# Kernel optimization log

Hardware: AMD Instinct MI355X
Metric: run time of the kernel (lower is better)

Reference implementation:

```python
import jax, jax.numpy as jnp
import numpy as np

EPS = 1e-5

def conv3x3(x, w, b=None):
    # NCHW, OIHW, stride 1, padding 1
    y = jax.lax.conv_general_dilated(x, w, (1, 1), ((1, 1), (1, 1)),
                                     dimension_numbers=('NCHW', 'OIHW', 'NCHW'))
    if b is not None:
        y = y + b[None, :, None, None]
    return y

def batchnorm(x, g, b):
    # training-mode BN (PyTorch default): biased variance over (N,H,W)
    m = x.mean((0, 2, 3), keepdims=True)
    v = x.var((0, 2, 3), keepdims=True)
    return (x - m) * jax.lax.rsqrt(v + EPS) * g[None, :, None, None] + b[None, :, None, None]

def upsample2x_align_corners(x):
    # bilinear, align_corners=True, scale_factor=2
    def lerp_axis(a, Lin, axis):
        Lout = 2 * Lin
        c = jnp.arange(Lout, dtype=a.dtype) * (Lin - 1) / (Lout - 1)
        i0 = jnp.floor(c).astype(jnp.int32)
        i1 = jnp.minimum(i0 + 1, Lin - 1)
        w = c - i0.astype(a.dtype)
        shape = [1] * a.ndim
        shape[axis] = Lout
        w = w.reshape(shape)
        return jnp.take(a, i0, axis=axis) * (1 - w) + jnp.take(a, i1, axis=axis) * w
    x = lerp_axis(x, x.shape[2], 2)
    x = lerp_axis(x, x.shape[3], 3)
    return x

def deform_sample(x, offsets):
    # torchvision DeformConv2d v1 sampling: kernel 3x3, pad 1, offsets [B,18,H,W]
    # layout: per kernel point k (row-major), channels (2k, 2k+1) = (dy, dx)
    B, C, H, W = x.shape
    K = 9
    off = offsets.reshape(B, K, 2, H, W)
    ky, kx = jnp.meshgrid(jnp.arange(3) - 1, jnp.arange(3) - 1, indexing='ij')
    ky = ky.reshape(K).astype(x.dtype)
    kx = kx.reshape(K).astype(x.dtype)
    gy = jnp.arange(H, dtype=x.dtype)[None, None, :, None]
    gx = jnp.arange(W, dtype=x.dtype)[None, None, None, :]
    py = gy + ky[None, :, None, None] + off[:, :, 0]  # [B,K,H,W]
    px = gx + kx[None, :, None, None] + off[:, :, 1]
    y0 = jnp.floor(py)
    x0 = jnp.floor(px)
    wy = (py - y0)[:, None]  # [B,1,K,H,W]
    wx = (px - x0)[:, None]
    y0i = y0.astype(jnp.int32)
    x0i = x0.astype(jnp.int32)
    x_flat = x.reshape(B, C, H * W)
    def gather(yi, xi):
        valid = ((yi >= 0) & (yi < H) & (xi >= 0) & (xi < W))
        idx = jnp.clip(yi, 0, H - 1) * W + jnp.clip(xi, 0, W - 1)  # [B,K,H,W]
        g = jnp.take_along_axis(x_flat, idx.reshape(B, 1, K * H * W), axis=2)
        return g.reshape(B, C, K, H, W) * valid[:, None].astype(x.dtype)
    v00 = gather(y0i, x0i)
    v01 = gather(y0i, x0i + 1)
    v10 = gather(y0i + 1, x0i)
    v11 = gather(y0i + 1, x0i + 1)
    return (v00 * (1 - wy) * (1 - wx) + v01 * (1 - wy) * wx
            + v10 * wy * (1 - wx) + v11 * wy * wx)

def setup_inputs() -> dict:
    key = jax.random.key(0)
    ks = jax.random.split(key, 6)
    B, in_ch, skip_ch, out_ch = 4, 256, 128, 128
    Hs, Ws = 128, 128
    x = jax.random.normal(ks[0], (B, in_ch, Hs // 2, Ws // 2), jnp.float32)
    skip = jax.random.normal(ks[1], (B, skip_ch, Hs, Ws), jnp.float32)
    cat_ch = in_ch + skip_ch
    conv1_w = jax.random.normal(ks[2], (out_ch, cat_ch, 3, 3), jnp.float32) * (2.0 / (cat_ch * 9)) ** 0.5
    off_w = jax.random.normal(ks[3], (18, out_ch, 3, 3), jnp.float32) * 0.01
    off_b = jnp.zeros((18,), jnp.float32)
    def_w = jax.random.normal(ks[4], (out_ch, out_ch, 3, 3), jnp.float32) * (2.0 / (out_ch * 9)) ** 0.5
    def_b = jnp.zeros((out_ch,), jnp.float32)
    return {
        'x': x, 'skip': skip,
        'conv1_w': conv1_w,
        'bn1_g': jnp.ones((out_ch,), jnp.float32), 'bn1_b': jnp.zeros((out_ch,), jnp.float32),
        'off_w': off_w, 'off_b': off_b,
        'def_w': def_w, 'def_b': def_b,
        'bn2_g': jnp.ones((out_ch,), jnp.float32), 'bn2_b': jnp.zeros((out_ch,), jnp.float32),
    }

def reference(x, skip, conv1_w, bn1_g, bn1_b, off_w, off_b, def_w, def_b, bn2_g, bn2_b):
    xu = upsample2x_align_corners(x)
    dh = skip.shape[2] - xu.shape[2]
    dw = skip.shape[3] - xu.shape[3]
    if dh != 0 or dw != 0:
        xu = jnp.pad(xu, ((0, 0), (0, 0), (dh // 2, dh - dh // 2), (dw // 2, dw - dw // 2)))
    cat = jnp.concatenate([skip, xu], axis=1)
    h = jax.nn.relu(batchnorm(conv3x3(cat, conv1_w), bn1_g, bn1_b))
    offsets = conv3x3(h, off_w, off_b)  # [B,18,H,W]
    sampled = deform_sample(h, offsets)  # [B,C,9,H,W]
    O = def_w.shape[0]
    y = jnp.einsum('ock,bckhw->bohw', def_w.reshape(O, def_w.shape[1], 9), sampled)
    y = y + def_b[None, :, None, None]
    return jax.nn.relu(batchnorm(y, bn2_g, bn2_b))
```

## Files before the change

kernel.cpp:

```cpp
#include <hip/hip_runtime.h>
#include <hip/hip_bf16.h>

typedef __hip_bfloat16 bf16;
typedef __bf16 bf16x8 __attribute__((ext_vector_type(8)));
typedef __bf16 bf16x4 __attribute__((ext_vector_type(4)));
typedef float  f32x4  __attribute__((ext_vector_type(4)));

constexpr int NB   = 4;
constexpr int H    = 128;
constexpr int W    = 128;
constexpr int HW   = H * W;
constexpr int NPIX = NB * HW;
constexpr int CCAT = 384;
constexpr int CSKIP= 128;
constexpr int CIN  = 256;
constexpr int CO   = 128;
constexpr int HS   = 64;
constexpr int WP   = 130;
constexpr int K1   = 3456;
constexpr int KD   = 1152;
constexpr int NBORD= 2 * WP + 2 * (WP - 2);
constexpr float EPS = 1e-5f;

__device__ __forceinline__ float b2f(bf16 v){ return __bfloat162float(v); }
__device__ __forceinline__ bf16  f2b(float v){ return __float2bfloat16(v); }

__device__ __forceinline__ void async_copy16(const void* g, void* s){
    __builtin_amdgcn_global_load_lds((const __attribute__((address_space(1))) void*)g,
                                     (__attribute__((address_space(3))) void*)s, 16, 0, 0);
}

__device__ __forceinline__ void border_yx(int p, int& y, int& x){
    if (p < WP)             { y = 0;        x = p; }
    else if (p < 2 * WP)    { y = WP - 1;   x = p - WP; }
    else if (p < 2 * WP + (WP - 2)) { y = p - 2 * WP + 1;          x = 0; }
    else                    { y = p - (2 * WP + (WP - 2)) + 1;     x = WP - 1; }
}

__global__ void k_prep(float* __restrict__ sums, bf16* __restrict__ catp,
                       bf16* __restrict__ hp){
    int i = blockIdx.x * blockDim.x + threadIdx.x;
    int stride = gridDim.x * blockDim.x;
    for (int j = i; j < 512; j += stride) sums[j] = 0.f;
    const int nCat = NB * NBORD * CCAT;
    for (int j = i; j < nCat; j += stride){
        int c = j % CCAT, r = j / CCAT, p = r % NBORD, b = r / NBORD;
        int y, x; border_yx(p, y, x);
        catp[(((size_t)b * WP + y) * WP + x) * CCAT + c] = f2b(0.f);
    }
    const int nHp = NB * NBORD * CO;
    for (int j = i; j < nHp; j += stride){
        int c = j % CO, r = j / CO, p = r % NBORD, b = r / NBORD;
        int y, x; border_yx(p, y, x);
        hp[(((size_t)b * WP + y) * WP + x) * CO + c] = f2b(0.f);
    }
}

__global__ __launch_bounds__(256) void k_build_cat2(const float* __restrict__ x,
                                                    const float* __restrict__ skip,
                                                    bf16* __restrict__ catp){
    constexpr int TS = 66;
    __shared__ bf16 tile[128 * TS];
    int t  = threadIdx.x;
    int y  = blockIdx.x % H, b = blockIdx.x / H;
    int xx = t & 127, cp = t >> 7;

    float cy = (y * 63.0f) / 127.0f;
    int   y0 = (int)cy;
    int   y1 = min(y0 + 1, HS - 1);
    float wy = cy - y0;
    float cxf = (xx * 63.0f) / 127.0f;
    int   x0 = (int)cxf;
    int   x1 = min(x0 + 1, HS - 1);
    float wx = cxf - x0;

    bf16* orow = catp + (((size_t)b * WP + y + 1) * WP + 1) * CCAT;

    for (int chunk = 0; chunk < 6; chunk++){
        int cbase = chunk * 64;
        if (chunk >= 1) __syncthreads();
        if (chunk < 2){
            const float* sb = skip + ((size_t)(b * CSKIP + cbase + cp * 32) * H + y) * W;
#pragma unroll
            for (int i = 0; i < 32; i++)
                tile[xx * TS + cp * 32 + i] = f2b(sb[(size_t)i * HW + xx]);
        } else {
            int icb = (chunk - 2) * 64 + cp * 32;
            const float* xr0 = x + ((size_t)(b * CIN + icb) * HS + y0) * HS;
            const float* xr1 = x + ((size_t)(b * CIN + icb) * HS + y1) * HS;
#pragma unroll
            for (int i = 0; i < 32; i++){
                const float* r0 = xr0 + (size_t)i * HS * HS;
                const float* r1 = xr1 + (size_t)i * HS * HS;
                float v0 = r0[x0] * (1 - wx) + r0[x1] * wx;
                float v1 = r1[x0] * (1 - wx) + r1[x1] * wx;
                tile[xx * TS + cp * 32 + i] = f2b(v0 * (1 - wy) + v1 * wy);
            }
        }
        __syncthreads();
        int cc2 = (t & 31) * 2;
        int px0 = t >> 5;
#pragma unroll
        for (int pp = 0; pp < 16; pp++){
            int px = pp * 8 + px0;
            unsigned int v = *(const unsigned int*)&tile[px * TS + cc2];
            *(unsigned int*)&orow[(size_t)px * CCAT + cbase + cc2] = v;
        }
    }
}

__global__ void k_tr_all(const float* __restrict__ w1, const float* __restrict__ wo,
                         const float* __restrict__ wd,
                         bf16* __restrict__ wt1, bf16* __restrict__ wto,
                         bf16* __restrict__ wtd){
    int i = blockIdx.x * blockDim.x + threadIdx.x;
    if (i < CO * K1){
        int e  = i & 7;
        int l  = (i >> 3) & 63;
        int nb = (i >> 9) & 7;
        int ks = (i >> 12) & 1;
        int p  = i >> 13;
        int gp = p / 6, q = p - gp * 6;
        int ky = gp / 3, ci = gp - ky * 3;
        int kx = q >> 1, s64 = q & 1;
        int oc = nb * 16 + (l & 15);
        int ic = ci * 128 + s64 * 64 + ks * 32 + (l >> 4) * 8 + e;
        wt1[i] = f2b(w1[((oc * CCAT + ic) * 3 + ky) * 3 + kx]);
        return;
    }
    i -= CO * K1;
    if (i < 32 * KD){
        int e  = i & 7;
        int l  = (i >> 3) & 63;
        int wn = (i >> 9) & 1;
        int s  = (i >> 10) & 3;
        int kk = i >> 12;
        int ky = kk / 3, kx = kk - ky * 3;
        int oc = wn * 16 + (l & 15);
        int ic = s * 32 + (l >> 4) * 8 + e;
        wto[i] = (oc < 18) ? f2b(wo[((oc * CO + ic) * 3 + ky) * 3 + kx]) : f2b(0.f);
        return;
    }
    i -= 32 * KD;
    if (i < CO * KD){
        int e  = i & 7;
        int l  = (i >> 3) & 63;
        int ni = (i >> 9) & 3;
        int wn = (i >> 11) & 1;
        int ks = (i >> 12) & 1;
        int kc = i >> 13;
        int oc = wn * 64 + ni * 16 + (l & 15);
        int ic = (kc & 1) * 64 + ks * 32 + (l >> 4) * 8 + e;
        int kp = kc >> 1;
        wtd[i] = f2b(wd[(oc * CO + ic) * 9 + kp]);
    }
}

__global__ __launch_bounds__(256) void k_conv1_mfma(const bf16* __restrict__ catp,
                                                    const bf16* __restrict__ wbt,
                                                    bf16* __restrict__ hp,
                                                    float* __restrict__ sums){
    __shared__ unsigned short Ab[2][68 * 128];
    __shared__ float ps[256];
    int t = threadIdx.x;
    int l = t & 63, w = t >> 6;
    int half = blockIdx.x & 1;
    int y = (blockIdx.x >> 1) % H, b = blockIdx.x / (2 * H);
    int px0 = half * 64;

    int m = l & 15, quad = l >> 4;

    f32x4 acc[4][2];
#pragma unroll
    for (int i = 0; i < 4; i++)
#pragma unroll
        for (int j = 0; j < 2; j++) acc[i][j] = f32x4{0.f, 0.f, 0.f, 0.f};

    const size_t rowStride = (size_t)WP * CCAT;
    const char* wq = (const char*)wbt + w * 2048 + l * 16;

    bf16x8 bA[2][2], bB[2][2];

    {
        const bf16* Arow = catp + ((size_t)(b * WP) + y) * rowStride + (size_t)px0 * CCAT;
        for (int i = w; i < 17; i += 4){
            int G = i * 64 + l;
            int px = G >> 4, ol = G & 15;
            int osrc = ol ^ (px & 7);
            async_copy16(Arow + (size_t)px * CCAT + osrc * 8, &Ab[0][i * 512]);
        }
#pragma unroll
        for (int ks = 0; ks < 2; ks++)
#pragma unroll
            for (int ni = 0; ni < 2; ni++)
                bA[ks][ni] = *(const bf16x8*)(wq + ks * 8192 + ni * 1024);
    }
    __syncthreads();

#pragma unroll 1
    for (int g = 0; g < 9; g++){
        if (g < 8){
            int gn = g + 1;
            int kyn = gn / 3, cin = gn - kyn * 3;
            const bf16* Arow = catp + ((size_t)(b * WP) + y + kyn) * rowStride
                             + (size_t)px0 * CCAT + cin * 128;
            for (int i = w; i < 17; i += 4){
                int G = i * 64 + l;
                int px = G >> 4, ol = G & 15;
                int osrc = ol ^ (px & 7);
                async_copy16(Arow + (size_t)px * CCAT + osrc * 8, &Ab[gn & 1][i * 512]);
            }
        }
        const bf16x8* ap = (const bf16x8*)&Ab[g & 1][0];
        const char* wg = wq + (size_t)g * 6 * 16384;
#pragma unroll
        for (int j = 0; j < 6; j++){
            int kx = j >> 1, s64 = j & 1;
            const char* wnx = wg + (j + 1) * 16384;
            if (j & 1){
#pragma unroll
                for (int ks = 0; ks < 2; ks++)
#pragma unroll
                    for (int ni = 0; ni < 2; ni++)
                        bA[ks][ni] = *(const bf16x8*)(wnx + ks * 8192 + ni * 1024);
            } else {
#pragma unroll
                for (int ks = 0; ks < 2; ks++)
#pragma unroll
                    for (int ni = 0; ni < 2; ni++)
                        bB[ks][ni] = *(const bf16x8*)(wnx + ks * 8192 + ni * 1024);
            }
#pragma unroll
            for (int ks = 0; ks < 2; ks++){
                int s = s64 * 2 + ks;
                bf16x8 af[4];
#pragma unroll
                for (int mi = 0; mi < 4; mi++){
                    int pxk = mi * 16 + m + kx;
                    af[mi] = ap[pxk * 16 + ((s * 4 + quad) ^ (pxk & 7))];
                }
                if (j & 1){
#pragma unroll
                    for (int mi = 0; mi < 4; mi++)
#pragma unroll
                        for (int ni = 0; ni < 2; ni++)
                            acc[mi][ni] = __builtin_amdgcn_mfma_f32_16x16x32_bf16(
                                af[mi], bB[ks][ni], acc[mi][ni], 0, 0, 0);
                } else {
#pragma unroll
                    for (int mi = 0; mi < 4; mi++)
#pragma unroll
                        for (int ni = 0; ni < 2; ni++)
                            acc[mi][ni] = __builtin_amdgcn_mfma_f32_16x16x32_bf16(
                                af[mi], bA[ks][ni], acc[mi][ni], 0, 0, 0);
                }
            }
        }
        __syncthreads();
    }

    size_t obase = (((size_t)b * WP + y + 1) * WP + 1 + px0) * CO;
#pragma unroll
    for (int mi = 0; mi < 4; mi++){
        int p0 = mi * 16 + quad * 4;
#pragma unroll
        for (int ni = 0; ni < 2; ni++){
            int oc = w * 32 + ni * 16 + m;
#pragma unroll
            for (int r = 0; r < 4; r++)
                hp[obase + (size_t)(p0 + r) * CO + oc] = f2b(acc[mi][ni][r]);
        }
    }
    ps[t] = 0.f;
    __syncthreads();
#pragma unroll
    for (int ni = 0; ni < 2; ni++){
        int ch = w * 32 + ni * 16 + m;
        float s = 0.f, q2 = 0.f;
#pragma unroll
        for (int mi = 0; mi < 4; mi++)
#pragma unroll
            for (int r = 0; r < 4; r++){
                float v = acc[mi][ni][r];
                s += v; q2 += v * v;
            }
        s += __shfl_xor(s, 16); s += __shfl_xor(s, 32);
        q2 += __shfl_xor(q2, 16); q2 += __shfl_xor(q2, 32);
        if (quad == 0){
            atomicAdd(&ps[ch], s);
            atomicAdd(&ps[128 + ch], q2);
        }
    }
    __syncthreads();
    if (t < 128){
        atomicAdd(&sums[t],       ps[t]);
        atomicAdd(&sums[128 + t], ps[128 + t]);
    }
}

__global__ __launch_bounds__(256) void k_bn_apply_pad(bf16* __restrict__ t,
                                                      const float* __restrict__ sums,
                                                      const float* __restrict__ g,
                                                      const float* __restrict__ bb){
    __shared__ float ssc[256];
    int tt = threadIdx.x;
    if (tt < 128){
        float mean = sums[tt] / (float)NPIX;
        float var  = sums[128 + tt] / (float)NPIX - mean * mean;
        float scale = g[tt] * rsqrtf(var + EPS);
        ssc[tt]       = scale;
        ssc[128 + tt] = bb[tt] - mean * scale;
    }
    __syncthreads();
    int i = blockIdx.x * 256 + tt;
    if (i >= NPIX * CO) return;
    int c = i & 127;
    int pix = i >> 7;
    int xw = pix & 127, yh = (pix >> 7) & 127, b = pix >> 14;
    size_t a = (((size_t)b * WP + yh + 1) * WP + xw + 1) * CO + c;
    float v = b2f(t[a]) * ssc[c] + ssc[128 + c];
    t[a] = f2b(v > 0.f ? v : 0.f);
}

__global__ __launch_bounds__(256) void k_conv_off_mfma(const bf16* __restrict__ hp,
                                                       const bf16* __restrict__ wob,
                                                       const float* __restrict__ off_b,
                                                       bf16* __restrict__ offs){
    __shared__ unsigned short Ab[68 * 128];
    int t = threadIdx.x, l = t & 63, w = t >> 6;
    int half = blockIdx.x & 1;
    int y = (blockIdx.x >> 1) % H, b = blockIdx.x / (2 * H);
    int px0 = half * 64;
    int m = l & 15, quad = l >> 4;
    int wm = w & 1, wn = w >> 1;

    f32x4 acc[2];
#pragma unroll
    for (int i = 0; i < 2; i++) acc[i] = f32x4{0.f, 0.f, 0.f, 0.f};

    const size_t rowStrideH = (size_t)WP * CO;
    const char* wq = (const char*)wob + wn * 1024 + l * 16;

    for (int ky = 0; ky < 3; ky++){
        if (ky) __syncthreads();
        const bf16* Arow = hp + ((size_t)(b * WP) + y + ky) * rowStrideH
                         + (size_t)px0 * CO;
        for (int i = w; i < 17; i += 4){
            int G  = i * 64 + l;
            int px = G >> 4, ol = G & 15;
            int osrc = ol ^ (px & 7);
            async_copy16(Arow + (size_t)px * CO + osrc * 8, &Ab[i * 512]);
        }
        bf16x8 bfr[3][4];
#pragma unroll
        for (int kx = 0; kx < 3; kx++)
#pragma unroll
            for (int s = 0; s < 4; s++)
                bfr[kx][s] = *(const bf16x8*)(wq + (((ky * 3 + kx) * 4 + s) * 2048));
        __syncthreads();
        const bf16x8* ap = (const bf16x8*)Ab;
        for (int kx = 0; kx < 3; kx++){
#pragma unroll
            for (int s = 0; s < 4; s++){
#pragma unroll
                for (int mi = 0; mi < 2; mi++){
                    int pxk = wm * 32 + mi * 16 + m + kx;
                    bf16x8 af = ap[pxk * 16 + ((s * 4 + quad) ^ (pxk & 7))];
                    acc[mi] = __builtin_amdgcn_mfma_f32_16x16x32_bf16(af, bfr[kx][s], acc[mi], 0, 0, 0);
                }
            }
        }
    }
    int oc = wn * 16 + m;
    if (oc < 18){
        float bias = off_b[oc];
        int rowpix = b * HW + y * W + px0;
#pragma unroll
        for (int mi = 0; mi < 2; mi++){
            int p0 = wm * 32 + mi * 16 + quad * 4;
#pragma unroll
            for (int r = 0; r < 4; r++)
                offs[(size_t)(rowpix + p0 + r) * 18 + oc] = f2b(acc[mi][r] + bias);
        }
    }
}

__global__ __launch_bounds__(256) void k_deform_mfma(const bf16* __restrict__ hp,
                                                     const bf16* __restrict__ offs,
                                                     const bf16* __restrict__ wdb,
                                                     const float* __restrict__ def_b,
                                                     bf16* __restrict__ y,
                                                     float* __restrict__ sums){
    __shared__ unsigned short Ab[2][128 * 64];
    __shared__ int2   sc_yx[9 * 128];
    __shared__ float4 sc_w[9 * 128];
    __shared__ float  ps[256];

    int t = threadIdx.x, l = t & 63, w = t >> 6;
    int yrow = blockIdx.x % H, b = blockIdx.x / H;
    int rowpix = b * HW + yrow * W;

    for (int idx = t; idx < 9 * 128; idx += 256){
        int kp = idx >> 7, px = idx & 127;
        float dy = b2f(offs[(size_t)(rowpix + px) * 18 + 2 * kp]);
        float dx = b2f(offs[(size_t)(rowpix + px) * 18 + 2 * kp + 1]);
        float py = yrow + (kp / 3 - 1) + dy;
        float pxx = px + (kp % 3 - 1) + dx;
        float fy = floorf(py), fx = floorf(pxx);
        float wy = py - fy, wx = pxx - fx;
        int y0 = (int)fy, x0 = (int)fx;
        bool vy0 = (y0 >= 0) && (y0 < H);
        bool vy1 = (y0 + 1 >= 0) && (y0 + 1 < H);
        bool vx0 = (x0 >= 0) && (x0 < W);
        bool vx1 = (x0 + 1 >= 0) && (x0 + 1 < W);
        int y0c = min(max(y0, 0), H - 1),     y1c = min(max(y0 + 1, 0), H - 1);
        int x0c = min(max(x0, 0), W - 1),     x1c = min(max(x0 + 1, 0), W - 1);
        sc_yx[idx] = make_int2(((y0c + 1) * WP) | (((y1c + 1) * WP) << 16),
                               (x0c + 1) | ((x1c + 1) << 16));
        sc_w[idx] = make_float4((1 - wy) * (1 - wx) * (float)(vy0 && vx0),
                                (1 - wy) * wx       * (float)(vy0 && vx1),
                                wy * (1 - wx)       * (float)(vy1 && vx0),
                                wy * wx             * (float)(vy1 && vx1));
    }
    __syncthreads();

    int m = l & 15, quad = l >> 4;
    int wm = w & 1, wn = w >> 1;
    int g = l >> 4, j = l & 15;

    f32x4 acc[4][4];
#pragma unroll
    for (int i = 0; i < 4; i++)
#pragma unroll
        for (int jj = 0; jj < 4; jj++) acc[i][jj] = f32x4{0.f, 0.f, 0.f, 0.f};

    const bf16* hpb = hp + (size_t)b * WP * WP * CO;
    const char* wq = (const char*)wdb + wn * 4096 + l * 16;

    auto GEN = [&](int kc, unsigned short* dst){
        int kp = kc >> 1, ch = (kc & 1) * 64;
        int cb = ch + j * 4;
#pragma unroll
        for (int p = 0; p < 8; p++){
            int px = w * 32 + g * 8 + p;
            int idx = kp * 128 + px;
            int2 yx = sc_yx[idx];
            float4 w4 = sc_w[idx];
            int r0 = yx.x & 0xffff, r1 = ((unsigned)yx.x) >> 16;
            int c0 = yx.y & 0xffff, c1 = ((unsigned)yx.y) >> 16;
            const bf16* base = hpb + cb;
            bf16x4 s00 = *(const bf16x4*)(base + (size_t)(r0 + c0) * CO);
            bf16x4 s01 = *(const bf16x4*)(base + (size_t)(r0 + c1) * CO);
            bf16x4 s10 = *(const bf16x4*)(base + (size_t)(r1 + c0) * CO);
            bf16x4 s11 = *(const bf16x4*)(base + (size_t)(r1 + c1) * CO);
            bf16x4 pv;
#pragma unroll
            for (int r = 0; r < 4; r++){
                float v = w4.x * (float)s00[r] + w4.y * (float)s01[r]
                        + w4.z * (float)s10[r] + w4.w * (float)s11[r];
                pv[r] = (__bf16)v;
            }
            int oct_sw = (j >> 1) ^ (px & 7);
            *(bf16x4*)&dst[px * 64 + oct_sw * 8 + (j & 1) * 4] = pv;
        }
    };

    GEN(0, &Ab[0][0]);

#pragma unroll 1
    for (int kc = 0; kc < 18; kc++){
        __syncthreads();
        bf16x8 bfr[2][4];
        const char* wk = wq + (size_t)kc * 16384;
#pragma unroll
        for (int ks = 0; ks < 2; ks++)
#pragma unroll
            for (int ni = 0; ni < 4; ni++)
                bfr[ks][ni] = *(const bf16x8*)(wk + ks * 8192 + ni * 1024);
        if (kc < 17) GEN(kc + 1, &Ab[(kc + 1) & 1][0]);

        const bf16x8* ap = (const bf16x8*)&Ab[kc & 1][0];
#pragma unroll
        for (int ks = 0; ks < 2; ks++){
            bf16x8 af[4];
#pragma unroll
            for (int mi = 0; mi < 4; mi++){
                int px = wm * 64 + mi * 16 + m;
                af[mi] = ap[px * 8 + ((ks * 4 + quad) ^ (px & 7))];
            }
#pragma unroll
            for (int mi = 0; mi < 4; mi++)
#pragma unroll
                for (int ni = 0; ni < 4; ni++)
                    acc[mi][ni] = __builtin_amdgcn_mfma_f32_16x16x32_bf16(
                        af[mi], bfr[ks][ni], acc[mi][ni], 0, 0, 0);
        }
    }
#pragma unroll
    for (int mi = 0; mi < 4; mi++){
        int p0 = wm * 64 + mi * 16 + quad * 4;
#pragma unroll
        for (int ni = 0; ni < 4; ni++){
            int oc = wn * 64 + ni * 16 + m;
            float bias = def_b[oc];
#pragma unroll
            for (int r = 0; r < 4; r++)
                y[(size_t)(rowpix + p0 + r) * CO + oc] = f2b(acc[mi][ni][r] + bias);
        }
    }
    ps[t] = 0.f;
    __syncthreads();
#pragma unroll
    for (int ni = 0; ni < 4; ni++){
        int ch = wn * 64 + ni * 16 + m;
        float bias = def_b[ch];
        float s = 0.f, q = 0.f;
#pragma unroll
        for (int mi = 0; mi < 4; mi++)
#pragma unroll
            for (int r = 0; r < 4; r++){
                float v = acc[mi][ni][r] + bias;
                s += v; q += v * v;
            }
        s += __shfl_xor(s, 16); s += __shfl_xor(s, 32);
        q += __shfl_xor(q, 16); q += __shfl_xor(q, 32);
        if (quad == 0){
            atomicAdd(&ps[ch], s);
            atomicAdd(&ps[128 + ch], q);
        }
    }
    __syncthreads();
    if (t < 128){
        atomicAdd(&sums[t],       ps[t]);
        atomicAdd(&sums[128 + t], ps[128 + t]);
    }
}

__global__ __launch_bounds__(256) void k_final(const bf16* __restrict__ yb,
                                               const float* __restrict__ sums,
                                               const float* __restrict__ g,
                                               const float* __restrict__ bb,
                                               float* __restrict__ out){
    __shared__ unsigned short tile[128 * 129];
    __shared__ float ssc[256];
    int t = threadIdx.x;
    if (t < 128){
        float mean = sums[t] / (float)NPIX;
        float var  = sums[128 + t] / (float)NPIX - mean * mean;
        float scale = g[t] * rsqrtf(var + EPS);
        ssc[t]       = scale;
        ssc[128 + t] = bb[t] - mean * scale;
    }
    int yrow = blockIdx.x % H, b = blockIdx.x / H;
    int rowbase = b * HW + yrow * W;
    const unsigned short* src = (const unsigned short*)yb;
    for (int it = 0; it < 64; it++){
        int idx = it * 256 + t;
        int c = idx & 127, px = idx >> 7;
        tile[px * 129 + c] = src[(size_t)(rowbase + px) * CO + c];
    }
    __syncthreads();
    for (int it = 0; it < 64; it++){
        int idx = it * 256 + t;
        int xw = idx & 127, o = idx >> 7;
        unsigned short u = tile[xw * 129 + o];
        float v = (float)(*(const __bf16*)&u);
        v = v * ssc[o] + ssc[128 + o];
        out[(((size_t)b * CO + o) * H + yrow) * W + xw] = v > 0.f ? v : 0.f;
    }
}

extern "C" void kernel_launch(void* const* d_in, const int* in_sizes, int n_in,
                              void* d_out, int out_size, void* d_ws, size_t ws_size,
                              hipStream_t stream){
    const float* x      = (const float*)d_in[0];
    const float* skip   = (const float*)d_in[1];
    const float* conv1w = (const float*)d_in[2];
    const float* bn1g   = (const float*)d_in[3];
    const float* bn1b   = (const float*)d_in[4];
    const float* offw   = (const float*)d_in[5];
    const float* offb   = (const float*)d_in[6];
    const float* defw   = (const float*)d_in[7];
    const float* defb   = (const float*)d_in[8];
    const float* bn2g   = (const float*)d_in[9];
    const float* bn2b   = (const float*)d_in[10];
    float* out = (float*)d_out;

    char* ws = (char*)d_ws;
    size_t off_bytes = 0;
    auto alloc = [&](size_t bytes) -> void* {
        void* p = ws + off_bytes;
        off_bytes += (bytes + 255) & ~(size_t)255;
        return p;
    };
    const size_t catp_elems = (size_t)NB * WP * WP * CCAT;
    const size_t hp_elems   = (size_t)NB * WP * WP * CO;
    bf16*  catp  = (bf16*) alloc(catp_elems * 2 + 2048);
    bf16*  hp    = (bf16*) alloc(hp_elems * 2 + 2048);
    bf16*  offs  = (bf16*) alloc((size_t)NPIX * 18 * 2);
    bf16*  yb    = (bf16*) alloc((size_t)NPIX * CO * 2);
    bf16*  wbt   = (bf16*) alloc((size_t)CO * K1 * 2 + 32768);
    bf16*  wob   = (bf16*) alloc((size_t)32 * KD * 2);
    bf16*  wdb   = (bf16*) alloc((size_t)CO * KD * 2);
    float* sums  = (float*)alloc(512 * 4);
    float* sums1 = sums;
    float* sums2 = sums + 256;

    k_prep<<<1024, 256, 0, stream>>>(sums, catp, hp);

    k_build_cat2<<<NB * H, 256, 0, stream>>>(x, skip, catp);

    const int ntr = CO * K1 + 32 * KD + CO * KD;
    k_tr_all<<<(ntr + 255) / 256, 256, 0, stream>>>(conv1w, offw, defw, wbt, wob, wdb);

    k_conv1_mfma<<<NB * H * 2, 256, 0, stream>>>(catp, wbt, hp, sums1);

    k_bn_apply_pad<<<(NPIX * CO + 255) / 256, 256, 0, stream>>>(hp, sums1, bn1g, bn1b);

    k_conv_off_mfma<<<NB * H * 2, 256, 0, stream>>>(hp, wob, offb, offs);

    k_deform_mfma<<<NB * H, 256, 0, stream>>>(hp, offs, wdb, defb, yb, sums2);

    k_final<<<NB * H, 256, 0, stream>>>(yb, sums2, bn2g, bn2b, out);
}
```

Before: 332.6 us.

## Fuse BN1 apply into offset conv and merge setup kernels into one launch

Merges the prep, concat-build and weight-transpose kernels into a single setup launch. Removes the standalone BN1 apply pass: the offset convolution now normalizes and ReLUs the raw conv1 output while staging it into LDS, and writes the normalized center row to a new buffer that the deform kernel reads. It also widens the LDS XOR swizzle from 8 to 16 slots in both convs. This cuts launches and one full read-modify-write of the conv1 activation, at the cost of an extra workspace buffer, synchronous loads instead of async LDS copies in the offset conv, and the new buffer's border relying on zero-filled memory.

Measured after the change: 314.5 us (median of 2 runs). 1.06x faster.

```diff
diff --git a/kernel.cpp b/kernel.cpp
--- a/kernel.cpp
+++ b/kernel.cpp
@@ -22,6 +22,10 @@
 constexpr int NBORD= 2 * WP + 2 * (WP - 2);
 constexpr float EPS = 1e-5f;
 
+constexpr int NTR  = CO * K1 + 32 * KD + CO * KD;
+constexpr int NCATB= NB * NBORD * CCAT;
+constexpr int NHPB = NB * NBORD * CO;
+
 __device__ __forceinline__ float b2f(bf16 v){ return __bfloat162float(v); }
 __device__ __forceinline__ bf16  f2b(float v){ return __float2bfloat16(v); }
 
@@ -37,112 +41,101 @@
     else                    { y = p - (2 * WP + (WP - 2)) + 1;     x = WP - 1; }
 }
 
-__global__ void k_prep(float* __restrict__ sums, bf16* __restrict__ catp,
-                       bf16* __restrict__ hp){
-    int i = blockIdx.x * blockDim.x + threadIdx.x;
-    int stride = gridDim.x * blockDim.x;
-    for (int j = i; j < 512; j += stride) sums[j] = 0.f;
-    const int nCat = NB * NBORD * CCAT;
-    for (int j = i; j < nCat; j += stride){
-        int c = j % CCAT, r = j / CCAT, p = r % NBORD, b = r / NBORD;
-        int y, x; border_yx(p, y, x);
-        catp[(((size_t)b * WP + y) * WP + x) * CCAT + c] = f2b(0.f);
-    }
-    const int nHp = NB * NBORD * CO;
-    for (int j = i; j < nHp; j += stride){
-        int c = j % CO, r = j / CO, p = r % NBORD, b = r / NBORD;
-        int y, x; border_yx(p, y, x);
-        hp[(((size_t)b * WP + y) * WP + x) * CO + c] = f2b(0.f);
-    }
-}
-
-__global__ __launch_bounds__(256) void k_build_cat2(const float* __restrict__ x,
-                                                    const float* __restrict__ skip,
-                                                    bf16* __restrict__ catp){
+__global__ __launch_bounds__(256) void k_setup(const float* __restrict__ x,
+                                               const float* __restrict__ skip,
+                                               const float* __restrict__ w1,
+                                               const float* __restrict__ wo,
+                                               const float* __restrict__ wd,
+                                               float* __restrict__ sums,
+                                               bf16* __restrict__ catp,
+                                               bf16* __restrict__ hp,
+                                               bf16* __restrict__ wt1,
+                                               bf16* __restrict__ wto,
+                                               bf16* __restrict__ wtd){
     constexpr int TS = 66;
     __shared__ bf16 tile[128 * TS];
-    int t  = threadIdx.x;
-    int y  = blockIdx.x % H, b = blockIdx.x / H;
-    int xx = t & 127, cp = t >> 7;
-
-    float cy = (y * 63.0f) / 127.0f;
-    int   y0 = (int)cy;
-    int   y1 = min(y0 + 1, HS - 1);
-    float wy = cy - y0;
-    float cxf = (xx * 63.0f) / 127.0f;
-    int   x0 = (int)cxf;
-    int   x1 = min(x0 + 1, HS - 1);
-    float wx = cxf - x0;
-
-    bf16* orow = catp + (((size_t)b * WP + y + 1) * WP + 1) * CCAT;
-
-    for (int chunk = 0; chunk < 6; chunk++){
-        int cbase = chunk * 64;
-        if (chunk >= 1) __syncthreads();
-        if (chunk < 2){
-            const float* sb = skip + ((size_t)(b * CSKIP + cbase + cp * 32) * H + y) * W;
-#pragma unroll
-            for (int i = 0; i < 32; i++)
-                tile[xx * TS + cp * 32 + i] = f2b(sb[(size_t)i * HW + xx]);
-        } else {
-            int icb = (chunk - 2) * 64 + cp * 32;
-            const float* xr0 = x + ((size_t)(b * CIN + icb) * HS + y0) * HS;
-            const float* xr1 = x + ((size_t)(b * CIN + icb) * HS + y1) * HS;
-#pragma unroll
-            for (int i = 0; i < 32; i++){
-                const float* r0 = xr0 + (size_t)i * HS * HS;
-                const float* r1 = xr1 + (size_t)i * HS * HS;
-                float v0 = r0[x0] * (1 - wx) + r0[x1] * wx;
-                float v1 = r1[x0] * (1 - wx) + r1[x1] * wx;
-                tile[xx * TS + cp * 32 + i] = f2b(v0 * (1 - wy) + v1 * wy);
-            }
-        }
-        __syncthreads();
-        int cc2 = (t & 31) * 2;
-        int px0 = t >> 5;
-#pragma unroll
-        for (int pp = 0; pp < 16; pp++){
-            int px = pp * 8 + px0;
-            unsigned int v = *(const unsigned int*)&tile[px * TS + cc2];
-            *(unsigned int*)&orow[(size_t)px * CCAT + cbase + cc2] = v;
-        }
-    }
-}
-
-__global__ void k_tr_all(const float* __restrict__ w1, const float* __restrict__ wo,
-                         const float* __restrict__ wd,
-                         bf16* __restrict__ wt1, bf16* __restrict__ wto,
-                         bf16* __restrict__ wtd){
-    int i = blockIdx.x * blockDim.x + threadIdx.x;
-    if (i < CO * K1){
-        int e  = i & 7;
-        int l  = (i >> 3) & 63;
-        int nb = (i >> 9) & 7;
-        int ks = (i >> 12) & 1;
-        int p  = i >> 13;
-        int gp = p / 6, q = p - gp * 6;
-        int ky = gp / 3, ci = gp - ky * 3;
-        int kx = q >> 1, s64 = q & 1;
-        int oc = nb * 16 + (l & 15);
-        int ic = ci * 128 + s64 * 64 + ks * 32 + (l >> 4) * 8 + e;
-        wt1[i] = f2b(w1[((oc * CCAT + ic) * 3 + ky) * 3 + kx]);
+    int t = threadIdx.x;
+
+    if (blockIdx.x < NB * H){
+        int y  = blockIdx.x % H, b = blockIdx.x / H;
+        int xx = t & 127, cp = t >> 7;
+
+        float cy = (y * 63.0f) / 127.0f;
+        int   y0 = (int)cy;
+        int   y1 = min(y0 + 1, HS - 1);
+        float wy = cy - y0;
+        float cxf = (xx * 63.0f) / 127.0f;
+        int   x0 = (int)cxf;
+        int   x1 = min(x0 + 1, HS - 1);
+        float wx = cxf - x0;
+
+        bf16* orow = catp + (((size_t)b * WP + y + 1) * WP + 1) * CCAT;
+
+        for (int chunk = 0; chunk < 6; chunk++){
+            int cbase = chunk * 64;
+            if (chunk >= 1) __syncthreads();
+            if (chunk < 2){
+                const float* sb = skip + ((size_t)(b * CSKIP + cbase + cp * 32) * H + y) * W;
+#pragma unroll
+                for (int i = 0; i < 32; i++)
+                    tile[xx * TS + cp * 32 + i] = f2b(sb[(size_t)i * HW + xx]);
+            } else {
+                int icb = (chunk - 2) * 64 + cp * 32;
+                const float* xr0 = x + ((size_t)(b * CIN + icb) * HS + y0) * HS;
+                const float* xr1 = x + ((size_t)(b * CIN + icb) * HS + y1) * HS;
+#pragma unroll
+                for (int i = 0; i < 32; i++){
+                    const float* r0 = xr0 + (size_t)i * HS * HS;
+                    const float* r1 = xr1 + (size_t)i * HS * HS;
+                    float v0 = r0[x0] * (1 - wx) + r0[x1] * wx;
+                    float v1 = r1[x0] * (1 - wx) + r1[x1] * wx;
+                    tile[xx * TS + cp * 32 + i] = f2b(v0 * (1 - wy) + v1 * wy);
+                }
+            }
+            __syncthreads();
+            int cc2 = (t & 31) * 2;
+            int px0 = t >> 5;
+#pragma unroll
+            for (int pp = 0; pp < 16; pp++){
+                int px = pp * 8 + px0;
+                unsigned int v = *(const unsigned int*)&tile[px * TS + cc2];
+                *(unsigned int*)&orow[(size_t)px * CCAT + cbase + cc2] = v;
+            }
+        }
         return;
     }
-    i -= CO * K1;
-    if (i < 32 * KD){
-        int e  = i & 7;
-        int l  = (i >> 3) & 63;
-        int wn = (i >> 9) & 1;
-        int s  = (i >> 10) & 3;
-        int kk = i >> 12;
-        int ky = kk / 3, kx = kk - ky * 3;
-        int oc = wn * 16 + (l & 15);
-        int ic = s * 32 + (l >> 4) * 8 + e;
-        wto[i] = (oc < 18) ? f2b(wo[((oc * CO + ic) * 3 + ky) * 3 + kx]) : f2b(0.f);
-        return;
-    }
-    i -= 32 * KD;
-    if (i < CO * KD){
+
+    int idx = (blockIdx.x - NB * H) * 256 + t;
+    if (idx < NTR){
+        int i = idx;
+        if (i < CO * K1){
+            int e  = i & 7;
+            int l  = (i >> 3) & 63;
+            int nb = (i >> 9) & 7;
+            int ks = (i >> 12) & 1;
+            int p  = i >> 13;
+            int gp = p / 6, q = p - gp * 6;
+            int ky = gp / 3, ci = gp - ky * 3;
+            int kx = q >> 1, s64 = q & 1;
+            int oc = nb * 16 + (l & 15);
+            int ic = ci * 128 + s64 * 64 + ks * 32 + (l >> 4) * 8 + e;
+            wt1[i] = f2b(w1[((oc * CCAT + ic) * 3 + ky) * 3 + kx]);
+            return;
+        }
+        i -= CO * K1;
+        if (i < 32 * KD){
+            int e  = i & 7;
+            int l  = (i >> 3) & 63;
+            int wn = (i >> 9) & 1;
+            int s  = (i >> 10) & 3;
+            int kk = i >> 12;
+            int ky = kk / 3, kx = kk - ky * 3;
+            int oc = wn * 16 + (l & 15);
+            int ic = s * 32 + (l >> 4) * 8 + e;
+            wto[i] = (oc < 18) ? f2b(wo[((oc * CO + ic) * 3 + ky) * 3 + kx]) : f2b(0.f);
+            return;
+        }
+        i -= 32 * KD;
         int e  = i & 7;
         int l  = (i >> 3) & 63;
         int ni = (i >> 9) & 3;
@@ -153,6 +146,22 @@
         int ic = (kc & 1) * 64 + ks * 32 + (l >> 4) * 8 + e;
         int kp = kc >> 1;
         wtd[i] = f2b(wd[(oc * CO + ic) * 9 + kp]);
+        return;
+    }
+    idx -= NTR;
+    if (idx < 512){ sums[idx] = 0.f; return; }
+    idx -= 512;
+    if (idx < NCATB){
+        int c = idx % CCAT, r = idx / CCAT, p = r % NBORD, b = r / NBORD;
+        int y, xw; border_yx(p, y, xw);
+        catp[(((size_t)b * WP + y) * WP + xw) * CCAT + c] = f2b(0.f);
+        return;
+    }
+    idx -= NCATB;
+    if (idx < NHPB){
+        int c = idx % CO, r = idx / CO, p = r % NBORD, b = r / NBORD;
+        int y, xw; border_yx(p, y, xw);
+        hp[(((size_t)b * WP + y) * WP + xw) * CO + c] = f2b(0.f);
     }
 }
 
@@ -186,7 +195,7 @@
         for (int i = w; i < 17; i += 4){
             int G = i * 64 + l;
             int px = G >> 4, ol = G & 15;
-            int osrc = ol ^ (px & 7);
+            int osrc = ol ^ (px & 15);
             async_copy16(Arow + (size_t)px * CCAT + osrc * 8, &Ab[0][i * 512]);
         }
 #pragma unroll
@@ -207,7 +216,7 @@
             for (int i = w; i < 17; i += 4){
                 int G = i * 64 + l;
                 int px = G >> 4, ol = G & 15;
-                int osrc = ol ^ (px & 7);
+                int osrc = ol ^ (px & 15);
                 async_copy16(Arow + (size_t)px * CCAT + osrc * 8, &Ab[gn & 1][i * 512]);
             }
         }
@@ -237,7 +246,7 @@
 #pragma unroll
                 for (int mi = 0; mi < 4; mi++){
                     int pxk = mi * 16 + m + kx;
-                    af[mi] = ap[pxk * 16 + ((s * 4 + quad) ^ (pxk & 7))];
+                    af[mi] = ap[pxk * 16 + ((s * 4 + quad) ^ (pxk & 15))];
                 }
                 if (j & 1){
 #pragma unroll
@@ -298,36 +307,23 @@
     }
 }
 
-__global__ __launch_bounds__(256) void k_bn_apply_pad(bf16* __restrict__ t,
-                                                      const float* __restrict__ sums,
-                                                      const float* __restrict__ g,
-                                                      const float* __restrict__ bb){
-    __shared__ float ssc[256];
-    int tt = threadIdx.x;
-    if (tt < 128){
-        float mean = sums[tt] / (float)NPIX;
-        float var  = sums[128 + tt] / (float)NPIX - mean * mean;
-        float scale = g[tt] * rsqrtf(var + EPS);
-        ssc[tt]       = scale;
-        ssc[128 + tt] = bb[tt] - mean * scale;
-    }
-    __syncthreads();
-    int i = blockIdx.x * 256 + tt;
-    if (i >= NPIX * CO) return;
-    int c = i & 127;
-    int pix = i >> 7;
-    int xw = pix & 127, yh = (pix >> 7) & 127, b = pix >> 14;
-    size_t a = (((size_t)b * WP + yh + 1) * WP + xw + 1) * CO + c;
-    float v = b2f(t[a]) * ssc[c] + ssc[128 + c];
-    t[a] = f2b(v > 0.f ? v : 0.f);
-}
-
 __global__ __launch_bounds__(256) void k_conv_off_mfma(const bf16* __restrict__ hp,
                                                        const bf16* __restrict__ wob,
                                                        const float* __restrict__ off_b,
-                                                       bf16* __restrict__ offs){
+                                                       const float* __restrict__ sums,
+                                                       const float* __restrict__ bn_g,
+                                                       const float* __restrict__ bn_b,
+                                                       bf16* __restrict__ offs,
+                                                       bf16* __restrict__ hq){
     __shared__ unsigned short Ab[68 * 128];
+    __shared__ float2 ssc[128];
     int t = threadIdx.x, l = t & 63, w = t >> 6;
+    if (t < 128){
+        float mean = sums[t] / (float)NPIX;
+        float var  = sums[128 + t] / (float)NPIX - mean * mean;
+        float sc   = bn_g[t] * rsqrtf(var + EPS);
+        ssc[t] = make_float2(sc, bn_b[t] - mean * sc);
+    }
     int half = blockIdx.x & 1;
     int y = (blockIdx.x >> 1) % H, b = blockIdx.x / (2 * H);
     int px0 = half * 64;
@@ -340,16 +336,33 @@
 
     const size_t rowStrideH = (size_t)WP * CO;
     const char* wq = (const char*)wob + wn * 1024 + l * 16;
+    __syncthreads();
 
     for (int ky = 0; ky < 3; ky++){
         if (ky) __syncthreads();
-        const bf16* Arow = hp + ((size_t)(b * WP) + y + ky) * rowStrideH
+        int row = y + ky;
+        const bf16* Arow = hp + ((size_t)(b * WP) + row) * rowStrideH
                          + (size_t)px0 * CO;
+        bool rowborder = (row == 0) || (row == WP - 1);
+        bf16* hqrow = hq + ((size_t)(b * WP) + row) * rowStrideH;
         for (int i = w; i < 17; i += 4){
             int G  = i * 64 + l;
             int px = G >> 4, ol = G & 15;
-            int osrc = ol ^ (px & 7);
-            async_copy16(Arow + (size_t)px * CO + osrc * 8, &Ab[i * 512]);
+            int osrc = ol ^ (px & 15);
+            int col = px0 + px;
+            bool zero = rowborder || (col == 0) || (col >= WP - 1);
+            bf16x8 raw = *(const bf16x8*)(Arow + (size_t)px * CO + osrc * 8);
+            bf16x8 outv;
+#pragma unroll
+            for (int e = 0; e < 8; e++){
+                float2 sb = ssc[osrc * 8 + e];
+                float v = (float)raw[e] * sb.x + sb.y;
+                v = v > 0.f ? v : 0.f;
+                outv[e] = zero ? (__bf16)0.f : (__bf16)v;
+            }
+            *(bf16x8*)&Ab[G * 8] = outv;
+            if (ky == 1 && col >= 1 && col <= 128)
+                *(bf16x8*)(hqrow + (size_t)col * CO + osrc * 8) = outv;
         }
         bf16x8 bfr[3][4];
 #pragma unroll
@@ -365,7 +378,7 @@
 #pragma unroll
                 for (int mi = 0; mi < 2; mi++){
                     int pxk = wm * 32 + mi * 16 + m + kx;
-                    bf16x8 af = ap[pxk * 16 + ((s * 4 + quad) ^ (pxk & 7))];
+                    bf16x8 af = ap[pxk * 16 + ((s * 4 + quad) ^ (pxk & 15))];
                     acc[mi] = __builtin_amdgcn_mfma_f32_16x16x32_bf16(af, bfr[kx][s], acc[mi], 0, 0, 0);
                 }
             }
@@ -385,7 +398,7 @@
     }
 }
 
-__global__ __launch_bounds__(256) void k_deform_mfma(const bf16* __restrict__ hp,
+__global__ __launch_bounds__(256) void k_deform_mfma(const bf16* __restrict__ hq,
                                                      const bf16* __restrict__ offs,
                                                      const bf16* __restrict__ wdb,
                                                      const float* __restrict__ def_b,
@@ -434,7 +447,7 @@
 #pragma unroll
         for (int jj = 0; jj < 4; jj++) acc[i][jj] = f32x4{0.f, 0.f, 0.f, 0.f};
 
-    const bf16* hpb = hp + (size_t)b * WP * WP * CO;
+    const bf16* hpb = hq + (size_t)b * WP * WP * CO;
     const char* wq = (const char*)wdb + wn * 4096 + l * 16;
 
     auto GEN = [&](int kc, unsigned short* dst){
@@ -597,6 +610,7 @@
     const size_t hp_elems   = (size_t)NB * WP * WP * CO;
     bf16*  catp  = (bf16*) alloc(catp_elems * 2 + 2048);
     bf16*  hp    = (bf16*) alloc(hp_elems * 2 + 2048);
+    bf16*  hq    = (bf16*) alloc(hp_elems * 2 + 2048);
     bf16*  offs  = (bf16*) alloc((size_t)NPIX * 18 * 2);
     bf16*  yb    = (bf16*) alloc((size_t)NPIX * CO * 2);
     bf16*  wbt   = (bf16*) alloc((size_t)CO * K1 * 2 + 32768);
@@ -606,20 +620,18 @@
     float* sums1 = sums;
     float* sums2 = sums + 256;
 
-    k_prep<<<1024, 256, 0, stream>>>(sums, catp, hp);
-
-    k_build_cat2<<<NB * H, 256, 0, stream>>>(x, skip, catp);
-
-    const int ntr = CO * K1 + 32 * KD + CO * KD;
-    k_tr_all<<<(ntr + 255) / 256, 256, 0, stream>>>(conv1w, offw, defw, wbt, wob, wdb);
+    const int nflat = NTR + 512 + NCATB + NHPB;
+    const int setup_blocks = NB * H + (nflat + 255) / 256;
+
+    k_setup<<<setup_blocks, 256, 0, stream>>>(x, skip, conv1w, offw, defw,
+                                              sums, catp, hp, wbt, wob, wdb);
 
     k_conv1_mfma<<<NB * H * 2, 256, 0, stream>>>(catp, wbt, hp, sums1);
 
-    k_bn_apply_pad<<<(NPIX * CO + 255) / 256, 256, 0, stream>>>(hp, sums1, bn1g, bn1b);
-
-    k_conv_off_mfma<<<NB * H * 2, 256, 0, stream>>>(hp, wob, offb, offs);
-
-    k_deform_mfma<<<NB * H, 256, 0, stream>>>(hp, offs, wdb, defb, yb, sums2);
+    k_conv_off_mfma<<<NB * H * 2, 256, 0, stream>>>(hp, wob, offb, sums1,
+                                                    bn1g, bn1b, offs, hq);
+
+    k_deform_mfma<<<NB * H, 256, 0, stream>>>(hq, offs, wdb, defb, yb, sums2);
 
     k_final<<<NB * H, 256, 0, stream>>>(yb, sums2, bn2g, bn2b, out);
 }
```
